# Performance work log

Hardware: AMD Instinct MI355X
Metric: run time of the kernel (lower is better)

Reference implementation:

```python
import jax, jax.numpy as jnp
import numpy as np

N, E = 50000, 800000
F_IN, HID, HEADS, OUT, NG = 128, 32, 4, 64, 64
HD = HID * HEADS  # 128


def gat_layer(x, src, dst, W, a_s, a_d, b, heads, out_c):
    n = x.shape[0]
    h = (x @ W).reshape(n, heads, out_c)                      # [N,H,C]
    al_s = jnp.einsum('nhc,hc->nh', h, a_s)                   # [N,H]
    al_d = jnp.einsum('nhc,hc->nh', h, a_d)
    e = jax.nn.leaky_relu(al_s[src] + al_d[dst], 0.2)         # [E,H]
    m = jax.ops.segment_max(e, dst, num_segments=n)
    ex = jnp.exp(e - m[dst])
    s = jax.ops.segment_sum(ex, dst, num_segments=n)
    alpha = ex / (s[dst] + 1e-16)                             # [E,H]
    msg = h[src] * alpha[:, :, None]                          # [E,H,C]
    out = jax.ops.segment_sum(msg, dst, num_segments=n)       # [N,H,C]
    return out.reshape(n, heads * out_c) + b


def batchnorm(x, g, be, eps=1e-5):
    mu = x.mean(0)
    var = x.var(0)
    return (x - mu) * jax.lax.rsqrt(var + eps) * g + be


def setup_inputs():
    key = jax.random.key(0)
    ks = jax.random.split(key, 32)
    inp = {}
    inp['x'] = jax.random.normal(ks[0], (N, F_IN), dtype=jnp.float32)
    inp['edge_index'] = jax.random.randint(ks[1], (2, E), 0, N, dtype=jnp.int64)
    inp['batch_ids'] = jnp.sort(jax.random.randint(ks[2], (N,), 0, NG, dtype=jnp.int64))
    dims = [(F_IN, HEADS, HID), (HD, HEADS, HID), (HD, HEADS, HID), (HD, 1, OUT)]
    for i, (din, h, c) in enumerate(dims):
        sc = 1.0 / np.sqrt(din)
        inp[f'W{i}'] = jax.random.normal(ks[3 + 4 * i], (din, h * c), dtype=jnp.float32) * sc
        inp[f'as{i}'] = jax.random.normal(ks[4 + 4 * i], (h, c), dtype=jnp.float32) * 0.1
        inp[f'ad{i}'] = jax.random.normal(ks[5 + 4 * i], (h, c), dtype=jnp.float32) * 0.1
        inp[f'b{i}'] = jnp.zeros((h * c,), dtype=jnp.float32)
    for i in range(3):
        inp[f'g{i}'] = jnp.ones((HD,), dtype=jnp.float32)
        inp[f'be{i}'] = jnp.zeros((HD,), dtype=jnp.float32)
    return inp


def reference(x, edge_index, batch_ids,
              W0, as0, ad0, b0, W1, as1, ad1, b1,
              W2, as2, ad2, b2, W3, as3, ad3, b3,
              g0, be0, g1, be1, g2, be2):
    # add self-loops (PyG GATConv default)
    loop = jnp.arange(N, dtype=edge_index.dtype)
    src = jnp.concatenate([edge_index[0], loop])
    dst = jnp.concatenate([edge_index[1], loop])

    h = x
    layers = [(W0, as0, ad0, b0, g0, be0), (W1, as1, ad1, b1, g1, be1),
              (W2, as2, ad2, b2, g2, be2)]
    for (W, a_s, a_d, b, g, be) in layers:
        h = gat_layer(h, src, dst, W, a_s, a_d, b, HEADS, HID)
        h = jax.nn.elu(batchnorm(h, g, be))
        # dropout p=0.6 is identity at inference
    h = gat_layer(h, src, dst, W3, as3, ad3, b3, 1, OUT)     # [N,OUT]

    # global mean pool over graphs
    ones = jnp.ones((N,), dtype=h.dtype)
    cnt = jax.ops.segment_sum(ones, batch_ids, num_segments=NG)
    summed = jax.ops.segment_sum(h, batch_ids, num_segments=NG)
    return summed / jnp.maximum(cnt, 1.0)[:, None]           # [NG,OUT]
```

## Files before the change

kernel.cpp:

```cpp
#include <hip/hip_runtime.h>

#define DEVINL __device__ __forceinline__

constexpr int N_NODES = 50000;
constexpr int E_EDGES = 800000;
constexpr int HD      = 128;
constexpr int NG      = 64;
constexpr int OUTC    = 64;
constexpr int NPAR    = 22;
constexpr int PAR_TOTAL = 3*(16384+3*128) + (8192+3*64) + 6*128;
constexpr int WT_TOTAL = 3*128*128 + 64*128;
constexpr int NB      = (N_NODES + 1023) / 1024;
constexpr int EBC     = 2048;
constexpr int NBLKC   = (E_EDGES + EBC - 1) / EBC;
constexpr int BNSLOTS = 16;
constexpr int PREP_BLOCKS = (PAR_TOTAL + WT_TOTAL + 255) / 256;

typedef _Float16 half8_t __attribute__((ext_vector_type(8)));
typedef _Float16 half4_t __attribute__((ext_vector_type(4)));
typedef float    float4_t __attribute__((ext_vector_type(4)));

DEVINL float bf2f(unsigned short u){
  union { unsigned int i; float f; } v; v.i = ((unsigned int)u) << 16; return v.f;
}
DEVINL float lrelu(float v){ return v > 0.f ? v : 0.2f * v; }

struct PtrTab { const void* p[NPAR]; int off[NPAR + 1]; };

__global__ __launch_bounds__(256) void k_prep(PtrTab tab,
                       const unsigned short* __restrict__ x,
                       const int* __restrict__ ei, int* __restrict__ flags,
                       float* __restrict__ dst,
                       const void* __restrict__ W0, const void* __restrict__ W1,
                       const void* __restrict__ W2, const void* __restrict__ W3,
                       _Float16* __restrict__ wt16, int* __restrict__ btot){
  __shared__ int s_f32, s_i64;
  __shared__ int cnt[NB];
  int t = threadIdx.x, blk = blockIdx.x;
  if (t == 0){ s_f32 = 0; s_i64 = 1; }
  if (t < NB) cnt[t] = 0;
  __syncthreads();
  for (int i = t; i < 2048; i += 256){
    float v = bf2f(x[i]);
    if (!(fabsf(v) < 1e4f)) s_f32 = 1;
  }
  for (int i = t; i < 512; i += 256){
    if (ei[2 * i + 1] != 0) s_i64 = 0;
  }
  __syncthreads();
  const int f = s_f32, i64 = s_i64;
  if (blk == 0 && t == 0){ flags[0] = i64; flags[1] = f; }

  int i = blk * 256 + t;
  if (i < PAR_TOTAL){
    int k = 0;
    while (tab.off[k + 1] <= i) k++;
    int j = i - tab.off[k];
    dst[i] = f ? ((const float*)tab.p[k])[j] : bf2f(((const unsigned short*)tab.p[k])[j]);
  } else {
    int w = i - PAR_TOTAL;
    if (w < WT_TOTAL){
      const void* W; int base, Mt;
      if (w < 49152){ int l = w >> 14; base = w & 16383; Mt = 128; W = (l == 0) ? W0 : (l == 1 ? W1 : W2); }
      else { base = w - 49152; Mt = 64; W = W3; }
      int nn = base >> 7, k = base & 127;
      float val = f ? ((const float*)W)[(size_t)k * Mt + nn]
                    : bf2f(((const unsigned short*)W)[(size_t)k * Mt + nn]);
      wt16[w] = (_Float16)val;
    }
  }

  if (blk < NBLKC){
    int e0 = blk * EBC;
    #pragma unroll
    for (int j = 0; j < EBC / 256; j++){
      int e = e0 + t + j * 256;
      if (e < E_EDGES){
        int d = ei[(size_t)(E_EDGES + e) << i64];
        atomicAdd(&cnt[d >> 10], 1);
      }
    }
    __syncthreads();
    if (t < NB && cnt[t] > 0) atomicAdd(&btot[t], cnt[t]);
  }
}

__global__ __launch_bounds__(256) void k_binscatter(const int* __restrict__ ei,
                      const int* __restrict__ flags, const int* __restrict__ btot,
                      int* __restrict__ curg, unsigned int* __restrict__ ebuf2){
  __shared__ int cnt[NB];
  __shared__ int cur[NB];
  __shared__ int cb[NB];
  int t = threadIdx.x, blk = blockIdx.x;
  if (t < NB) cnt[t] = 0;
  __syncthreads();
  int f = flags[0];
  int e0 = blk * EBC;
  unsigned int my[EBC / 256];
  #pragma unroll
  for (int j = 0; j < EBC / 256; j++){
    int e = e0 + t + j * 256;
    my[j] = 0xFFFFFFFFu;
    if (e < E_EDGES){
      int s = ei[(size_t)e << f];
      int d = ei[(size_t)(E_EDGES + e) << f];
      my[j] = (unsigned int)s | ((unsigned int)d << 16);
      atomicAdd(&cnt[d >> 10], 1);
    }
  }
  __syncthreads();
  if (t == 0){
    int run = 0;
    for (int b = 0; b < NB; b++){ cb[b] = run; run += btot[b]; }
  }
  __syncthreads();
  if (t < NB && cnt[t] > 0) cur[t] = cb[t] + atomicAdd(&curg[t], cnt[t]);
  __syncthreads();
  #pragma unroll
  for (int j = 0; j < EBC / 256; j++){
    unsigned int pk = my[j];
    if (pk != 0xFFFFFFFFu){
      int p = atomicAdd(&cur[pk >> 26], 1);
      ebuf2[p] = pk;
    }
  }
}

__global__ __launch_bounds__(256) void k_csrD(const unsigned int* __restrict__ ebuf2,
                      const int* __restrict__ btot, int* __restrict__ offs,
                      int* __restrict__ ssrc, int n){
  __shared__ int hist[1024];
  __shared__ int wsum[256];
  __shared__ int cb[NB + 1];
  int t = threadIdx.x, b = blockIdx.x;
  int nbase = b << 10;
  if (t == 0){
    int run = 0;
    for (int bb = 0; bb < NB; bb++){ cb[bb] = run; run += btot[bb]; }
    cb[NB] = run;
  }
  for (int i = t; i < 1024; i += 256) hist[i] = 0;
  __syncthreads();
  int s0 = cb[b], s1 = cb[b + 1];
  for (int i = s0 + t; i < s1; i += 256){
    unsigned int pk = ebuf2[i];
    atomicAdd(&hist[(int)(pk >> 16) - nbase], 1);
  }
  __syncthreads();
  int base4 = t * 4;
  int v0 = hist[base4], v1 = hist[base4 + 1], v2 = hist[base4 + 2], v3 = hist[base4 + 3];
  int s = v0 + v1 + v2 + v3;
  wsum[t] = s; __syncthreads();
  for (int off = 1; off < 256; off <<= 1){
    int x2 = (t >= off) ? wsum[t - off] : 0;
    __syncthreads();
    wsum[t] += x2;
    __syncthreads();
  }
  int run = s0 + wsum[t] - s;
  int node = nbase + base4;
  if (node < n) offs[node] = run;  hist[base4] = run;  run += v0;
  if (node + 1 < n) offs[node + 1] = run;  hist[base4 + 1] = run;  run += v1;
  if (node + 2 < n) offs[node + 2] = run;  hist[base4 + 2] = run;  run += v2;
  if (node + 3 < n) offs[node + 3] = run;  hist[base4 + 3] = run;
  if (b == NB - 1 && t == 255) offs[n] = s1;
  __syncthreads();
  for (int i = s0 + t; i < s1; i += 256){
    unsigned int pk = ebuf2[i];
    int p = atomicAdd(&hist[(int)(pk >> 16) - nbase], 1);
    ssrc[p] = (int)(pk & 0xFFFFu);
  }
}

template<int MT, bool FIRST>
__global__ __launch_bounds__(256) void k_gemm(
    const void* __restrict__ Ain, const int* __restrict__ flags,
    const float* __restrict__ bnslots,
    const float* __restrict__ g, const float* __restrict__ be,
    const _Float16* __restrict__ Wt16,
    const float* __restrict__ a_s, const float* __restrict__ a_d,
    _Float16* __restrict__ h16, float* __restrict__ als, float* __restrict__ ald,
    int n){
  __shared__ _Float16 AhL[64 * 136];
  __shared__ _Float16 WtL[MT * 72];
  __shared__ float scale[128], shift[128];
  const int t = threadIdx.x;
  const int rowBase = blockIdx.x * 64;
  if (!FIRST){
    if (t < 128){
      float s = 0.f, q = 0.f;
      #pragma unroll
      for (int sl = 0; sl < BNSLOTS; sl++){
        s += bnslots[sl * 256 + t];
        q += bnslots[sl * 256 + 128 + t];
      }
      float inv_n = 1.f / (float)n;
      float mu = s * inv_n;
      float var = q * inv_n - mu * mu;
      float sc = g[t] * rsqrtf(var + 1e-5f);
      scale[t] = sc; shift[t] = be[t] - mu * sc;
    }
    __syncthreads();
  }
  for (int f = t; f < 64 * 16; f += 256){
    int r = f >> 4, c8 = (f & 15) << 3;
    int row = rowBase + r;
    float v[8];
    if (row < n){
      if (FIRST){
        if (flags[1]){
          float4 x0 = *(const float4*)((const float*)Ain + (size_t)row * 128 + c8);
          float4 x1 = *(const float4*)((const float*)Ain + (size_t)row * 128 + c8 + 4);
          v[0]=x0.x; v[1]=x0.y; v[2]=x0.z; v[3]=x0.w;
          v[4]=x1.x; v[5]=x1.y; v[6]=x1.z; v[7]=x1.w;
        } else {
          const unsigned short* xp = (const unsigned short*)Ain + (size_t)row * 128 + c8;
          ushort4 u0 = *(const ushort4*)xp; ushort4 u1 = *(const ushort4*)(xp + 4);
          v[0]=bf2f(u0.x); v[1]=bf2f(u0.y); v[2]=bf2f(u0.z); v[3]=bf2f(u0.w);
          v[4]=bf2f(u1.x); v[5]=bf2f(u1.y); v[6]=bf2f(u1.z); v[7]=bf2f(u1.w);
        }
      } else {
        half8_t a8 = *(const half8_t*)((const _Float16*)Ain + (size_t)row * 128 + c8);
        #pragma unroll
        for (int j = 0; j < 8; j++){
          float xv = (float)a8[j] * scale[c8 + j] + shift[c8 + j];
          v[j] = xv > 0.f ? xv : (__expf(xv) - 1.f);
        }
      }
    } else {
      #pragma unroll
      for (int j = 0; j < 8; j++) v[j] = 0.f;
    }
    half8_t h;
    #pragma unroll
    for (int j = 0; j < 8; j++) h[j] = (_Float16)v[j];
    *(half8_t*)&AhL[r * 136 + c8] = h;
  }
  const int lane = t & 63;
  const int m = lane & 15, quad = lane >> 4;
  const int band = (t >> 6) * 16;
  float4_t acc[MT / 16];
  #pragma unroll
  for (int ct = 0; ct < MT / 16; ct++) acc[ct] = (float4_t){0.f, 0.f, 0.f, 0.f};
  #pragma unroll
  for (int kh = 0; kh < 2; kh++){
    __syncthreads();
    for (int f = t; f < MT * 8; f += 256){
      int nn = f >> 3, c8 = (f & 7) << 3;
      *(half8_t*)&WtL[nn * 72 + c8] = *(const half8_t*)&Wt16[nn * 128 + kh * 64 + c8];
    }
    __syncthreads();
    half8_t a0 = *(half8_t*)&AhL[(band + m) * 136 + kh * 64 + quad * 8];
    half8_t a1 = *(half8_t*)&AhL[(band + m) * 136 + kh * 64 + 32 + quad * 8];
    #pragma unroll
    for (int ct = 0; ct < MT / 16; ct++){
      half8_t b0 = *(half8_t*)&WtL[(ct * 16 + m) * 72 + quad * 8];
      half8_t b1 = *(half8_t*)&WtL[(ct * 16 + m) * 72 + 32 + quad * 8];
      acc[ct] = __builtin_amdgcn_mfma_f32_16x16x32_f16(a0, b0, acc[ct], 0, 0, 0);
      acc[ct] = __builtin_amdgcn_mfma_f32_16x16x32_f16(a1, b1, acc[ct], 0, 0, 0);
    }
  }
  __syncthreads();
  #pragma unroll
  for (int ct = 0; ct < MT / 16; ct++)
    #pragma unroll
    for (int rg = 0; rg < 4; rg++)
      AhL[(band + quad * 4 + rg) * 136 + ct * 16 + m] = (_Float16)acc[ct][rg];
  __syncthreads();
  int r = t >> 2, q = t & 3;
  int row = rowBase + r;
  if (MT == 128){
    if (row < n){
      half8_t h0 = *(half8_t*)&AhL[r * 136 + q * 32];
      half8_t h1 = *(half8_t*)&AhL[r * 136 + q * 32 + 8];
      half8_t h2 = *(half8_t*)&AhL[r * 136 + q * 32 + 16];
      half8_t h3 = *(half8_t*)&AhL[r * 136 + q * 32 + 24];
      float pas = 0.f, pad = 0.f;
      #pragma unroll
      for (int j = 0; j < 8; j++){
        pas += (float)h0[j] * a_s[q * 32 + j]      + (float)h1[j] * a_s[q * 32 + 8 + j]
             + (float)h2[j] * a_s[q * 32 + 16 + j] + (float)h3[j] * a_s[q * 32 + 24 + j];
        pad += (float)h0[j] * a_d[q * 32 + j]      + (float)h1[j] * a_d[q * 32 + 8 + j]
             + (float)h2[j] * a_d[q * 32 + 16 + j] + (float)h3[j] * a_d[q * 32 + 24 + j];
      }
      als[(size_t)row * 4 + q] = pas;
      ald[(size_t)row * 4 + q] = pad;
      _Float16* hp = h16 + (size_t)row * 128 + q * 32;
      *(half8_t*)hp = h0; *(half8_t*)(hp + 8) = h1;
      *(half8_t*)(hp + 16) = h2; *(half8_t*)(hp + 24) = h3;
    }
  } else {
    half8_t h0 = *(half8_t*)&AhL[r * 136 + q * 16];
    half8_t h1 = *(half8_t*)&AhL[r * 136 + q * 16 + 8];
    float pas = 0.f, pad = 0.f;
    #pragma unroll
    for (int j = 0; j < 8; j++){
      pas += (float)h0[j] * a_s[q * 16 + j] + (float)h1[j] * a_s[q * 16 + 8 + j];
      pad += (float)h0[j] * a_d[q * 16 + j] + (float)h1[j] * a_d[q * 16 + 8 + j];
    }
    pas += __shfl_xor(pas, 1); pas += __shfl_xor(pas, 2);
    pad += __shfl_xor(pad, 1); pad += __shfl_xor(pad, 2);
    if (row < n){
      _Float16* hp = h16 + (size_t)row * 64 + q * 16;
      *(half8_t*)hp = h0; *(half8_t*)(hp + 8) = h1;
      if (q == 0){ als[row] = pas; ald[row] = pad; }
    }
  }
}

template<int H, int C, int MODE>
__global__ __launch_bounds__(256) void k_attn(const _Float16* __restrict__ h16,
                      const float* __restrict__ als, const float* __restrict__ ald,
                      const int* __restrict__ offs, const int* __restrict__ ssrc,
                      const float* __restrict__ bias,
                      _Float16* __restrict__ a16out, float* __restrict__ bnout,
                      const int* __restrict__ bids, const int* __restrict__ flags,
                      float* __restrict__ psum, int* __restrict__ gcnt, int n){
  constexpr int HC = H * C;
  constexpr int CPL = HC / 16;
  int t = threadIdx.x;
  int nib  = t >> 4;
  int node = blockIdx.x * 16 + nib;
  int sub  = t & 15;
  int c0   = sub * CPL;
  int head = c0 / C;

  float ald_h = ald[(size_t)node * H + head];
  float acc[CPL];
  float ssum;
  {
    float w = __expf(lrelu(als[(size_t)node * H + head] + ald_h));
    ssum = w;
    const _Float16* hp = h16 + (size_t)node * HC + c0;
    #pragma unroll
    for (int i = 0; i < CPL; i++) acc[i] = w * (float)hp[i];
  }
  int beg = offs[node];
  int deg = offs[node + 1] - beg;
  int j = 0;
  for (; j + 8 <= deg; j += 8){
    int ss[8]; float al[8]; float w[8];
    #pragma unroll
    for (int u = 0; u < 8; u++) ss[u] = ssrc[beg + j + u];
    #pragma unroll
    for (int u = 0; u < 8; u++) al[u] = als[(size_t)ss[u] * H + head];
    if constexpr (CPL == 8){
      half8_t v[8];
      #pragma unroll
      for (int u = 0; u < 8; u++) v[u] = *(const half8_t*)(h16 + (size_t)ss[u] * HC + c0);
      #pragma unroll
      for (int u = 0; u < 8; u++){ w[u] = __expf(lrelu(al[u] + ald_h)); ssum += w[u]; }
      #pragma unroll
      for (int i = 0; i < 8; i++){
        float a = 0.f;
        #pragma unroll
        for (int u = 0; u < 8; u++) a += w[u] * (float)v[u][i];
        acc[i] += a;
      }
    } else {
      half4_t v[8];
      #pragma unroll
      for (int u = 0; u < 8; u++) v[u] = *(const half4_t*)(h16 + (size_t)ss[u] * HC + c0);
      #pragma unroll
      for (int u = 0; u < 8; u++){ w[u] = __expf(lrelu(al[u] + ald_h)); ssum += w[u]; }
      #pragma unroll
      for (int i = 0; i < 4; i++){
        float a = 0.f;
        #pragma unroll
        for (int u = 0; u < 8; u++) a += w[u] * (float)v[u][i];
        acc[i] += a;
      }
    }
  }
  for (; j + 4 <= deg; j += 4){
    int s0 = ssrc[beg + j], s1 = ssrc[beg + j + 1];
    int s2 = ssrc[beg + j + 2], s3 = ssrc[beg + j + 3];
    float al0 = als[(size_t)s0 * H + head], al1 = als[(size_t)s1 * H + head];
    float al2 = als[(size_t)s2 * H + head], al3 = als[(size_t)s3 * H + head];
    float w0 = __expf(lrelu(al0 + ald_h)), w1 = __expf(lrelu(al1 + ald_h));
    float w2 = __expf(lrelu(al2 + ald_h)), w3 = __expf(lrelu(al3 + ald_h));
    ssum += (w0 + w1) + (w2 + w3);
    if constexpr (CPL == 8){
      half8_t v0 = *(const half8_t*)(h16 + (size_t)s0 * HC + c0);
      half8_t v1 = *(const half8_t*)(h16 + (size_t)s1 * HC + c0);
      half8_t v2 = *(const half8_t*)(h16 + (size_t)s2 * HC + c0);
      half8_t v3 = *(const half8_t*)(h16 + (size_t)s3 * HC + c0);
      #pragma unroll
      for (int i = 0; i < 8; i++)
        acc[i] += w0 * (float)v0[i] + w1 * (float)v1[i]
                + w2 * (float)v2[i] + w3 * (float)v3[i];
    } else {
      half4_t v0 = *(const half4_t*)(h16 + (size_t)s0 * HC + c0);
      half4_t v1 = *(const half4_t*)(h16 + (size_t)s1 * HC + c0);
      half4_t v2 = *(const half4_t*)(h16 + (size_t)s2 * HC + c0);
      half4_t v3 = *(const half4_t*)(h16 + (size_t)s3 * HC + c0);
      #pragma unroll
      for (int i = 0; i < 4; i++)
        acc[i] += w0 * (float)v0[i] + w1 * (float)v1[i]
                + w2 * (float)v2[i] + w3 * (float)v3[i];
    }
  }
  for (; j < deg; j++){
    int s0 = ssrc[beg + j];
    float w0 = __expf(lrelu(als[(size_t)s0 * H + head] + ald_h));
    ssum += w0;
    const _Float16* hp = h16 + (size_t)s0 * HC + c0;
    #pragma unroll
    for (int i = 0; i < CPL; i++) acc[i] += w0 * (float)hp[i];
  }
  float inv_s = 1.f / ssum;
  float v[CPL];
  #pragma unroll
  for (int i = 0; i < CPL; i++) v[i] = acc[i] * inv_s + bias[c0 + i];

  if constexpr (MODE == 0){
    _Float16* op = a16out + (size_t)node * HC + c0;
    half8_t o;
    #pragma unroll
    for (int i = 0; i < CPL; i++) o[i] = (_Float16)v[i];
    *(half8_t*)op = o;
    __shared__ float red[16][132];
    *(float4*)&red[nib][c0]     = make_float4(v[0], v[1], v[2], v[3]);
    *(float4*)&red[nib][c0 + 4] = make_float4(v[4], v[5], v[6], v[7]);
    __syncthreads();
    if (t < 128){
      float s = 0.f, q = 0.f;
      #pragma unroll
      for (int i = 0; i < 16; i++){ float x = red[i][t]; s += x; q += x * x; }
      int slot = blockIdx.x & (BNSLOTS - 1);
      atomicAdd(&bnout[slot * 256 + t], s);
      atomicAdd(&bnout[slot * 256 + 128 + t], q);
    }
  } else {
    __shared__ float pacc[2][64];
    __shared__ int pcnt[2];
    int f = flags[0];
    if (t < 128) pacc[t >> 6][t & 63] = 0.f;
    if (t < 2) pcnt[t] = 0;
    __syncthreads();
    int g  = (int)bids[(size_t)node << f];
    int g0 = (int)bids[(size_t)(blockIdx.x * 16) << f];
    int g1 = (int)bids[(size_t)(blockIdx.x * 16 + 15) << f];
    if (g1 - g0 <= 1){
      int gl = g - g0;
      #pragma unroll
      for (int i = 0; i < 4; i++) atomicAdd(&pacc[gl][c0 + i], v[i]);
      if (sub == 0) atomicAdd(&pcnt[gl], 1);
      __syncthreads();
      if (t < 128){
        int gl2 = t >> 6;
        if (pcnt[gl2] > 0) atomicAdd(&psum[(g0 + gl2) * 64 + (t & 63)], pacc[gl2][t & 63]);
      }
      if (t < 2 && pcnt[t] > 0) atomicAdd(&gcnt[g0 + t], pcnt[t]);
    } else {
      #pragma unroll
      for (int i = 0; i < 4; i++) atomicAdd(&psum[g * 64 + c0 + i], v[i]);
      if (sub == 0) atomicAdd(&gcnt[g], 1);
      __syncthreads();
    }
  }
}

__global__ void k_pool_fin(const float* __restrict__ psum, const int* __restrict__ gcnt,
                           float* __restrict__ out){
  int i = blockIdx.x * 256 + threadIdx.x;
  if (i >= NG * OUTC) return;
  int cnt = gcnt[i >> 6];
  out[i] = psum[i] / (float)(cnt > 1 ? cnt : 1);
}

extern "C" void kernel_launch(void* const* d_in, const int* in_sizes, int n_in,
                              void* d_out, int out_size, void* d_ws, size_t ws_size,
                              hipStream_t stream){
  const unsigned short* x    = (const unsigned short*)d_in[0];
  const int*            ei   = (const int*)d_in[1];
  const int*            bids = (const int*)d_in[2];

  char* p = (char*)d_ws;
  auto carve = [&](size_t bytes) -> void* {
    void* r = (void*)p; p += (bytes + 255) & ~size_t(255); return r;
  };
  _Float16* a16    = (_Float16*)carve((size_t)N_NODES * HD * 2);
  _Float16* h16    = (_Float16*)carve((size_t)N_NODES * HD * 2);
  float*    par    = (float*)carve((size_t)PAR_TOTAL * 4);
  _Float16* wt16   = (_Float16*)carve((size_t)WT_TOTAL * 2);
  float*    als    = (float*)carve((size_t)N_NODES * 4 * 4);
  float*    ald    = (float*)carve((size_t)N_NODES * 4 * 4);
  int*      offs   = (int*)carve((size_t)(N_NODES + 1) * 4);
  int*      ssrc   = (int*)carve((size_t)E_EDGES * 4);
  unsigned int* ebuf2 = (unsigned int*)carve((size_t)E_EDGES * 4);
  int*      flags  = (int*)carve(256);
  char*     zbeg   = p;
  int*      btot   = (int*)carve(256);
  int*      curg   = (int*)carve(256);
  float*    bnbuf  = (float*)carve((size_t)3 * BNSLOTS * 256 * 4);
  float*    psum   = (float*)carve(NG * OUTC * 4);
  int*      gcnt   = (int*)carve(256);
  size_t    zlen   = (size_t)(p - zbeg);

  PtrTab tab;
  int sizes[NPAR];
  for (int l = 0; l < 4; l++){
    int base = 3 + 4 * l;
    tab.p[4 * l + 0] = d_in[base + 0]; sizes[4 * l + 0] = (l < 3) ? 16384 : 8192;
    tab.p[4 * l + 1] = d_in[base + 1]; sizes[4 * l + 1] = (l < 3) ? 128 : 64;
    tab.p[4 * l + 2] = d_in[base + 2]; sizes[4 * l + 2] = (l < 3) ? 128 : 64;
    tab.p[4 * l + 3] = d_in[base + 3]; sizes[4 * l + 3] = (l < 3) ? 128 : 64;
  }
  for (int l = 0; l < 3; l++){
    tab.p[16 + 2 * l]     = d_in[19 + 2 * l];     sizes[16 + 2 * l] = 128;
    tab.p[16 + 2 * l + 1] = d_in[19 + 2 * l + 1]; sizes[16 + 2 * l + 1] = 128;
  }
  tab.off[0] = 0;
  for (int k = 0; k < NPAR; k++) tab.off[k + 1] = tab.off[k] + sizes[k];
  const float* pAS[4], *pAD[4], *pB[4], *pG[3], *pBE[3];
  for (int l = 0; l < 4; l++){
    pAS[l] = par + tab.off[4 * l + 1];
    pAD[l] = par + tab.off[4 * l + 2];
    pB[l]  = par + tab.off[4 * l + 3];
  }
  for (int l = 0; l < 3; l++){
    pG[l]  = par + tab.off[16 + 2 * l];
    pBE[l] = par + tab.off[16 + 2 * l + 1];
  }
  const _Float16* pWT[4] = { wt16, wt16 + 16384, wt16 + 32768, wt16 + 49152 };
  float* bnS[3];
  for (int l = 0; l < 3; l++) bnS[l] = bnbuf + (size_t)l * BNSLOTS * 256;

  hipMemsetAsync(zbeg, 0, zlen, stream);

  k_prep<<<PREP_BLOCKS, 256, 0, stream>>>(
      tab, x, ei, flags, par, d_in[3], d_in[7], d_in[11], d_in[15], wt16, btot);

  k_binscatter<<<NBLKC, 256, 0, stream>>>(ei, flags, btot, curg, ebuf2);
  k_csrD<<<NB, 256, 0, stream>>>(ebuf2, btot, offs, ssrc, N_NODES);

  int gemmBlocks = (N_NODES + 63) / 64;
  int attnBlocks = N_NODES / 16;

  k_gemm<128, true><<<gemmBlocks, 256, 0, stream>>>(
      (const void*)x, flags, nullptr, nullptr, nullptr,
      pWT[0], pAS[0], pAD[0], h16, als, ald, N_NODES);
  k_attn<4, 32, 0><<<attnBlocks, 256, 0, stream>>>(h16, als, ald, offs, ssrc, pB[0],
      a16, bnS[0], nullptr, nullptr, nullptr, nullptr, N_NODES);
  for (int l = 1; l < 3; l++){
    k_gemm<128, false><<<gemmBlocks, 256, 0, stream>>>(
        (const void*)a16, flags, bnS[l-1], pG[l-1], pBE[l-1],
        pWT[l], pAS[l], pAD[l], h16, als, ald, N_NODES);
    k_attn<4, 32, 0><<<attnBlocks, 256, 0, stream>>>(h16, als, ald, offs, ssrc, pB[l],
        a16, bnS[l], nullptr, nullptr, nullptr, nullptr, N_NODES);
  }
  k_gemm<64, false><<<gemmBlocks, 256, 0, stream>>>(
      (const void*)a16, flags, bnS[2], pG[2], pBE[2],
      pWT[3], pAS[3], pAD[3], h16, als, ald, N_NODES);
  k_attn<1, 64, 1><<<attnBlocks, 256, 0, stream>>>(h16, als, ald, offs, ssrc, pB[3],
      nullptr, nullptr, bids, flags, psum, gcnt, N_NODES);

  k_pool_fin<<<16, 256, 0, stream>>>(psum, gcnt, (float*)d_out);
}
```

Measured before the change: 419.7 us.

## Sort attention nodes by in-degree bucket to balance warp work

Builds a degree histogram in the CSR kernel, prefix-sums it in a tiny kernel, and scatters node ids into degree-bucketed order during the first GEMM. The three hidden-layer attention kernels then process nodes in that permuted order, so nodes of similar degree share a wavefront and divergence in the edge loop drops. It costs an extra launch, an atomic scatter, one more indirection per node, and writes to a16/BN outputs scattered rather than contiguous.

```diff
diff --git a/kernel.cpp b/kernel.cpp
--- a/kernel.cpp
+++ b/kernel.cpp
@@ -15,6 +15,7 @@
 constexpr int NBLKC   = (E_EDGES + EBC - 1) / EBC;
 constexpr int BNSLOTS = 16;
 constexpr int PREP_BLOCKS = (PAR_TOTAL + WT_TOTAL + 255) / 256;
+constexpr int DBINS   = 32;
 
 typedef _Float16 half8_t __attribute__((ext_vector_type(8)));
 typedef _Float16 half4_t __attribute__((ext_vector_type(4)));
@@ -128,10 +129,11 @@
 
 __global__ __launch_bounds__(256) void k_csrD(const unsigned int* __restrict__ ebuf2,
                       const int* __restrict__ btot, int* __restrict__ offs,
-                      int* __restrict__ ssrc, int n){
+                      int* __restrict__ ssrc, int* __restrict__ dbin, int n){
   __shared__ int hist[1024];
   __shared__ int wsum[256];
   __shared__ int cb[NB + 1];
+  __shared__ int dbl[DBINS];
   int t = threadIdx.x, b = blockIdx.x;
   int nbase = b << 10;
   if (t == 0){
@@ -139,6 +141,7 @@
     for (int bb = 0; bb < NB; bb++){ cb[bb] = run; run += btot[bb]; }
     cb[NB] = run;
   }
+  if (t < DBINS) dbl[t] = 0;
   for (int i = t; i < 1024; i += 256) hist[i] = 0;
   __syncthreads();
   int s0 = cb[b], s1 = cb[b + 1];
@@ -150,6 +153,13 @@
   int base4 = t * 4;
   int v0 = hist[base4], v1 = hist[base4 + 1], v2 = hist[base4 + 2], v3 = hist[base4 + 3];
   int s = v0 + v1 + v2 + v3;
+  {
+    int node = nbase + base4;
+    if (node < n)     atomicAdd(&dbl[min(v0, DBINS - 1)], 1);
+    if (node + 1 < n) atomicAdd(&dbl[min(v1, DBINS - 1)], 1);
+    if (node + 2 < n) atomicAdd(&dbl[min(v2, DBINS - 1)], 1);
+    if (node + 3 < n) atomicAdd(&dbl[min(v3, DBINS - 1)], 1);
+  }
   wsum[t] = s; __syncthreads();
   for (int off = 1; off < 256; off <<= 1){
     int x2 = (t >= off) ? wsum[t - off] : 0;
@@ -164,11 +174,19 @@
   if (node + 2 < n) offs[node + 2] = run;  hist[base4 + 2] = run;  run += v2;
   if (node + 3 < n) offs[node + 3] = run;  hist[base4 + 3] = run;
   if (b == NB - 1 && t == 255) offs[n] = s1;
+  if (t < DBINS && dbl[t] > 0) atomicAdd(&dbin[t], dbl[t]);
   __syncthreads();
   for (int i = s0 + t; i < s1; i += 256){
     unsigned int pk = ebuf2[i];
     int p = atomicAdd(&hist[(int)(pk >> 16) - nbase], 1);
     ssrc[p] = (int)(pk & 0xFFFFu);
+  }
+}
+
+__global__ void k_dperm(const int* __restrict__ dbin, int* __restrict__ dcur){
+  if (threadIdx.x == 0){
+    int run = 0;
+    for (int b = 0; b < DBINS; b++){ dcur[b] = run; run += dbin[b]; }
   }
 }
 
@@ -180,13 +198,23 @@
     const _Float16* __restrict__ Wt16,
     const float* __restrict__ a_s, const float* __restrict__ a_d,
     _Float16* __restrict__ h16, float* __restrict__ als, float* __restrict__ ald,
+    const int* __restrict__ offs, int* __restrict__ dcur, int* __restrict__ perm,
     int n){
   __shared__ _Float16 AhL[64 * 136];
   __shared__ _Float16 WtL[MT * 72];
   __shared__ float scale[128], shift[128];
   const int t = threadIdx.x;
   const int rowBase = blockIdx.x * 64;
-  if (!FIRST){
+  if (FIRST){
+    if (t < 64){
+      int node = rowBase + t;
+      if (node < n){
+        int deg = offs[node + 1] - offs[node];
+        int pos = atomicAdd(&dcur[min(deg, DBINS - 1)], 1);
+        perm[pos] = node;
+      }
+    }
+  } else {
     if (t < 128){
       float s = 0.f, q = 0.f;
       #pragma unroll
@@ -315,12 +343,13 @@
                       const float* __restrict__ bias,
                       _Float16* __restrict__ a16out, float* __restrict__ bnout,
                       const int* __restrict__ bids, const int* __restrict__ flags,
-                      float* __restrict__ psum, int* __restrict__ gcnt, int n){
+                      float* __restrict__ psum, int* __restrict__ gcnt,
+                      const int* __restrict__ perm, int n){
   constexpr int HC = H * C;
   constexpr int CPL = HC / 16;
   int t = threadIdx.x;
   int nib  = t >> 4;
-  int node = blockIdx.x * 16 + nib;
+  int node = (MODE == 0) ? perm[blockIdx.x * 16 + nib] : (blockIdx.x * 16 + nib);
   int sub  = t & 15;
   int c0   = sub * CPL;
   int head = c0 / C;
@@ -489,10 +518,13 @@
   int*      offs   = (int*)carve((size_t)(N_NODES + 1) * 4);
   int*      ssrc   = (int*)carve((size_t)E_EDGES * 4);
   unsigned int* ebuf2 = (unsigned int*)carve((size_t)E_EDGES * 4);
+  int*      perm   = (int*)carve((size_t)N_NODES * 4);
+  int*      dcur   = (int*)carve(256);
   int*      flags  = (int*)carve(256);
   char*     zbeg   = p;
   int*      btot   = (int*)carve(256);
   int*      curg   = (int*)carve(256);
+  int*      dbin   = (int*)carve(256);
   float*    bnbuf  = (float*)carve((size_t)3 * BNSLOTS * 256 * 4);
   float*    psum   = (float*)carve(NG * OUTC * 4);
   int*      gcnt   = (int*)carve(256);
@@ -533,28 +565,29 @@
       tab, x, ei, flags, par, d_in[3], d_in[7], d_in[11], d_in[15], wt16, btot);
 
   k_binscatter<<<NBLKC, 256, 0, stream>>>(ei, flags, btot, curg, ebuf2);
-  k_csrD<<<NB, 256, 0, stream>>>(ebuf2, btot, offs, ssrc, N_NODES);
+  k_csrD<<<NB, 256, 0, stream>>>(ebuf2, btot, offs, ssrc, dbin, N_NODES);
+  k_dperm<<<1, 64, 0, stream>>>(dbin, dcur);
 
   int gemmBlocks = (N_NODES + 63) / 64;
   int attnBlocks = N_NODES / 16;
 
   k_gemm<128, true><<<gemmBlocks, 256, 0, stream>>>(
       (const void*)x, flags, nullptr, nullptr, nullptr,
-      pWT[0], pAS[0], pAD[0], h16, als, ald, N_NODES);
+      pWT[0], pAS[0], pAD[0], h16, als, ald, offs, dcur, perm, N_NODES);
   k_attn<4, 32, 0><<<attnBlocks, 256, 0, stream>>>(h16, als, ald, offs, ssrc, pB[0],
-      a16, bnS[0], nullptr, nullptr, nullptr, nullptr, N_NODES);
+      a16, bnS[0], nullptr, nullptr, nullptr, nullptr, perm, N_NODES);
   for (int l = 1; l < 3; l++){
     k_gemm<128, false><<<gemmBlocks, 256, 0, stream>>>(
         (const void*)a16, flags, bnS[l-1], pG[l-1], pBE[l-1],
-        pWT[l], pAS[l], pAD[l], h16, als, ald, N_NODES);
+        pWT[l], pAS[l], pAD[l], h16, als, ald, nullptr, nullptr, nullptr, N_NODES);
     k_attn<4, 32, 0><<<attnBlocks, 256, 0, stream>>>(h16, als, ald, offs, ssrc, pB[l],
-        a16, bnS[l], nullptr, nullptr, nullptr, nullptr, N_NODES);
+        a16, bnS[l], nullptr, nullptr, nullptr, nullptr, perm, N_NODES);
   }
   k_gemm<64, false><<<gemmBlocks, 256, 0, stream>>>(
       (const void*)a16, flags, bnS[2], pG[2], pBE[2],
-      pWT[3], pAS[3], pAD[3], h16, als, ald, N_NODES);
+      pWT[3], pAS[3], pAD[3], h16, als, ald, nullptr, nullptr, nullptr, N_NODES);
   k_attn<1, 64, 1><<<attnBlocks, 256, 0, stream>>>(h16, als, ald, offs, ssrc, pB[3],
-      nullptr, nullptr, bids, flags, psum, gcnt, N_NODES);
+      nullptr, nullptr, bids, flags, psum, gcnt, nullptr, N_NODES);
 
   k_pool_fin<<<16, 256, 0, stream>>>(psum, gcnt, (float*)d_out);
 }
```

Result: slower. 550.4 us (+31.1%).
